# Performance work log

Hardware: AMD Instinct MI355X
Metric: run time of the kernel (lower is better)

Reference implementation:

```python
import jax, jax.numpy as jnp
import numpy as np

V, EMB, DU = 32000, 256, 512   # vocab_size, embedding_dim, dec_units
B, TIN, TOUT = 32, 64, 64      # batch, max_length_input, max_length_output


def setup_inputs() -> dict:
    key = jax.random.key(0)
    ks = jax.random.split(key, 12)
    s = 0.02  # init scale for params
    return {
        "inputs": jax.random.randint(ks[0], (B, TOUT), 0, V),
        "encoder_outputs": jax.random.normal(ks[1], (B, TIN, DU), dtype=jnp.float32),
        "h0": jax.random.normal(ks[2], (B, DU), dtype=jnp.float32),
        "c0": jax.random.normal(ks[3], (B, DU), dtype=jnp.float32),
        "emb": jax.random.normal(ks[4], (V, EMB), dtype=jnp.float32) * s,
        "Wq": jax.random.normal(ks[5], (EMB, DU), dtype=jnp.float32) * s,
        "bq": jnp.zeros((DU,), jnp.float32),
        "Wx": jax.random.normal(ks[6], (DU + EMB, 4 * DU), dtype=jnp.float32) * s,
        "Wh": jax.random.normal(ks[7], (DU, 4 * DU), dtype=jnp.float32) * s,
        "b_lstm": jnp.zeros((4 * DU,), jnp.float32),
        "Wfc": jax.random.normal(ks[8], (DU, V), dtype=jnp.float32) * s,
        "bfc": jnp.zeros((V,), jnp.float32),
    }


def _lstm(lstm_in, h0, c0, Wx, Wh, b):
    # lstm_in: [B, T, D]; keras LSTMCell gate order: i, f, g(cell), o
    def step(carry, xt):
        h, c = carry
        z = xt @ Wx + h @ Wh + b  # [B, 4*DU]
        i, f, g, o = jnp.split(z, 4, axis=-1)
        c = jax.nn.sigmoid(f) * c + jax.nn.sigmoid(i) * jnp.tanh(g)
        h = jax.nn.sigmoid(o) * jnp.tanh(c)
        return (h, c), h
    (h, c), hs = jax.lax.scan(step, (h0, c0), jnp.swapaxes(lstm_in, 0, 1))
    return jnp.swapaxes(hs, 0, 1), h, c  # [B, T, DU], [B, DU], [B, DU]


def reference(inputs, encoder_outputs, h0, c0, emb, Wq, bq, Wx, Wh, b_lstm, Wfc, bfc):
    x = emb[inputs]                                       # [B, Tout, EMB]
    q = x @ Wq + bq                                       # Luong query  [B, Tout, DU]
    scores = jnp.einsum('btd,bsd->bts', q, encoder_outputs)  # dot-product attention
    attn_w = jax.nn.softmax(scores, axis=-1)              # [B, Tout, Tin]
    att = jnp.einsum('bts,bsd->btd', attn_w, encoder_outputs)  # [B, Tout, DU]
    lstm_in = jnp.concatenate([att, x], axis=-1)          # [B, Tout, DU+EMB]
    hs, state_h, state_c = _lstm(lstm_in, h0, c0, Wx, Wh, b_lstm)
    logits = hs @ Wfc + bfc                               # [B, Tout, V]
    return logits, (state_h, state_c), attn_w
```

## Files before the change

### kernel.cpp

```cpp
#include <hip/hip_runtime.h>
#include <cstdint>

#define NB 32
#define TIN 64
#define TOUT 64
#define EMB 256
#define DU 512
#define VSZ 32000
#define BT 2048
#define G4 2048
#define KL 768

typedef __attribute__((ext_vector_type(4))) float f32x4;
typedef __attribute__((ext_vector_type(8))) short s16x8;

__device__ __forceinline__ unsigned short f2bf(float f){
  unsigned int u = __float_as_uint(f);
  u += 0x7fffu + ((u >> 16) & 1u);
  return (unsigned short)(u >> 16);
}

__global__ void k_embed(const int* __restrict__ toks, const float* __restrict__ emb,
                        unsigned short* __restrict__ x_bf, unsigned short* __restrict__ lstmin){
  int idx = blockIdx.x * 256 + threadIdx.x;
  int row = idx >> 8, e = idx & 255;
  int tok = toks[row];
  unsigned short h = f2bf(emb[tok * EMB + e]);
  x_bf[row * EMB + e] = h;
  lstmin[row * KL + DU + e] = h;
}

__global__ void k_h0cast(const float* __restrict__ h0, unsigned short* __restrict__ hbuf){
  int i = blockIdx.x * 256 + threadIdx.x;
  hbuf[i] = f2bf(h0[i]);
}

__global__ void k_enccast(const float* __restrict__ enc, unsigned short* __restrict__ enc_bf,
                          unsigned short* __restrict__ encT){
  int b = blockIdx.z, dt = blockIdx.x, st = blockIdx.y;
  __shared__ float tile[32][33];
  int tx = threadIdx.x & 31, ty = threadIdx.x >> 5;
  const float* eb = enc + b * TIN * DU;
  #pragma unroll
  for (int i = 0; i < 4; i++){
    int s = st*32 + ty + i*8, d = dt*32 + tx;
    float v = eb[s * DU + d];
    tile[ty + i*8][tx] = v;
    enc_bf[(b * TIN + s) * DU + d] = f2bf(v);
  }
  __syncthreads();
  #pragma unroll
  for (int i = 0; i < 4; i++){
    int d = dt*32 + ty + i*8, s = st*32 + tx;
    encT[(b * DU + d) * TIN + s] = f2bf(tile[tx][ty + i*8]);
  }
}

__global__ void k_transpose(const float* __restrict__ in, unsigned short* __restrict__ out, int R, int C){
  __shared__ float tile[32][33];
  int tx = threadIdx.x & 31, ty = threadIdx.x >> 5;
  int c0 = blockIdx.x * 32, r0 = blockIdx.y * 32;
  #pragma unroll
  for (int i = 0; i < 4; i++) tile[ty + i*8][tx] = in[(r0 + ty + i*8) * C + c0 + tx];
  __syncthreads();
  #pragma unroll
  for (int i = 0; i < 4; i++) out[(c0 + ty + i*8) * R + r0 + tx] = f2bf(tile[tx][ty + i*8]);
}

template<bool OUT_BF16, bool BIAS>
__global__ __launch_bounds__(256) void k_gemm_bt(const unsigned short* __restrict__ A,
                                                 const unsigned short* __restrict__ Bt,
                                                 const float* __restrict__ bias,
                                                 void* __restrict__ Cout, int M, int N, int K){
  __shared__ unsigned short As[128][72];
  __shared__ unsigned short Bs[128][72];
  const int tid = threadIdx.x;
  const int wave = tid >> 6, lane = tid & 63;
  const int l15 = lane & 15, quad = lane >> 4;
  const int m_base = blockIdx.y * 128, n_base = blockIdx.x * 128;
  const int wr = wave >> 1, wc = wave & 1;
  f32x4 acc[4][4] = {};
  const int srow = tid >> 3, schunk = (tid & 7) * 8;
  for (int k0 = 0; k0 < K; k0 += 64){
    #pragma unroll
    for (int rr = 0; rr < 4; rr++){
      int r = rr * 32 + srow;
      *(s16x8*)&As[r][schunk] = *(const s16x8*)&A[(size_t)(m_base + r) * K + k0 + schunk];
      *(s16x8*)&Bs[r][schunk] = *(const s16x8*)&Bt[(size_t)(n_base + r) * K + k0 + schunk];
    }
    __syncthreads();
    #pragma unroll
    for (int ks = 0; ks < 2; ks++){
      s16x8 af[4], bfm[4];
      #pragma unroll
      for (int mt = 0; mt < 4; mt++) af[mt]  = *(const s16x8*)&As[wr*64 + mt*16 + l15][ks*32 + quad*8];
      #pragma unroll
      for (int nt = 0; nt < 4; nt++) bfm[nt] = *(const s16x8*)&Bs[wc*64 + nt*16 + l15][ks*32 + quad*8];
      #pragma unroll
      for (int mt = 0; mt < 4; mt++)
        #pragma unroll
        for (int nt = 0; nt < 4; nt++)
          acc[mt][nt] = __builtin_amdgcn_mfma_f32_16x16x32_bf16(af[mt], bfm[nt], acc[mt][nt], 0, 0, 0);
    }
    __syncthreads();
  }
  #pragma unroll
  for (int mt = 0; mt < 4; mt++){
    #pragma unroll
    for (int nt = 0; nt < 4; nt++){
      int n = n_base + wc*64 + nt*16 + l15;
      float bv = BIAS ? bias[n] : 0.f;
      #pragma unroll
      for (int r = 0; r < 4; r++){
        int m = m_base + wr*64 + mt*16 + quad*4 + r;
        float v = acc[mt][nt][r] + bv;
        if (OUT_BF16) ((unsigned short*)Cout)[(size_t)m * N + n] = f2bf(v);
        else          ((float*)Cout)[(size_t)m * N + n] = v;
      }
    }
  }
}

__global__ __launch_bounds__(256) void k_gemm_lds(const unsigned short* __restrict__ A,
                                                  const unsigned short* __restrict__ Bt,
                                                  const float* __restrict__ bias,
                                                  float* __restrict__ Cout, int M, int N, int K){
  __shared__ unsigned short As[128 * 64];
  __shared__ unsigned short Bs[128 * 64];
  const int tid = threadIdx.x;
  const int wave = tid >> 6, lane = tid & 63;
  const int l15 = lane & 15, quad = lane >> 4;
  const int m_base = blockIdx.y * 128, n_base = blockIdx.x * 128;
  const int wr = wave >> 1, wc = wave & 1;
  f32x4 acc[4][4] = {};
  const int srow = lane >> 3;
  const int scol = (lane & 7) * 8;
  for (int k0 = 0; k0 < K; k0 += 64){
    #pragma unroll
    for (int i = 0; i < 4; i++){
      int ra = wave * 32 + i * 8;
      const unsigned short* ga = &A [(size_t)(m_base + ra + srow) * K + k0 + scol];
      const unsigned short* gb = &Bt[(size_t)(n_base + ra + srow) * K + k0 + scol];
      __builtin_amdgcn_global_load_lds((const __attribute__((address_space(1))) unsigned int*)ga,
                                       (__attribute__((address_space(3))) unsigned int*)&As[ra * 64],
                                       16, 0, 0);
      __builtin_amdgcn_global_load_lds((const __attribute__((address_space(1))) unsigned int*)gb,
                                       (__attribute__((address_space(3))) unsigned int*)&Bs[ra * 64],
                                       16, 0, 0);
    }
    __syncthreads();
    #pragma unroll
    for (int ks = 0; ks < 2; ks++){
      s16x8 af[4], bfm[4];
      #pragma unroll
      for (int mt = 0; mt < 4; mt++) af[mt]  = *(const s16x8*)&As[(wr*64 + mt*16 + l15) * 64 + ks*32 + quad*8];
      #pragma unroll
      for (int nt = 0; nt < 4; nt++) bfm[nt] = *(const s16x8*)&Bs[(wc*64 + nt*16 + l15) * 64 + ks*32 + quad*8];
      #pragma unroll
      for (int mt = 0; mt < 4; mt++)
        #pragma unroll
        for (int nt = 0; nt < 4; nt++)
          acc[mt][nt] = __builtin_amdgcn_mfma_f32_16x16x32_bf16(af[mt], bfm[nt], acc[mt][nt], 0, 0, 0);
    }
    __syncthreads();
  }
  #pragma unroll
  for (int mt = 0; mt < 4; mt++){
    #pragma unroll
    for (int nt = 0; nt < 4; nt++){
      int n = n_base + wc*64 + nt*16 + l15;
      float bv = bias[n];
      #pragma unroll
      for (int r = 0; r < 4; r++){
        int m = m_base + wr*64 + mt*16 + quad*4 + r;
        Cout[(size_t)m * N + n] = acc[mt][nt][r] + bv;
      }
    }
  }
}

__global__ __launch_bounds__(256) void k_attn(const unsigned short* __restrict__ q,
                                              const unsigned short* __restrict__ enc_bf,
                                              const unsigned short* __restrict__ encT,
                                              float* __restrict__ attn_out,
                                              unsigned short* __restrict__ lstmin){
  const int b = blockIdx.x;
  const int tid = threadIdx.x;
  const int wave = tid >> 6, lane = tid & 63;
  const int l15 = lane & 15, quad = lane >> 4;
  __shared__ unsigned short AB[2][64][136];
  __shared__ float ss[64][66];
  __shared__ unsigned short Ps[64][72];

  f32x4 acc[4] = {};
  for (int kc = 0; kc < 4; kc++){
    int k0 = kc * 128;
    #pragma unroll
    for (int i = 0; i < 4; i++){
      int idx = i * 256 + tid;
      int row = idx >> 4, ch = (idx & 15) * 8;
      *(s16x8*)&AB[0][row][ch] = *(const s16x8*)&q[(b*64 + row) * DU + k0 + ch];
      *(s16x8*)&AB[1][row][ch] = *(const s16x8*)&enc_bf[(b*64 + row) * DU + k0 + ch];
    }
    __syncthreads();
    #pragma unroll
    for (int ks = 0; ks < 4; ks++){
      s16x8 a = *(const s16x8*)&AB[0][wave*16 + l15][ks*32 + quad*8];
      #pragma unroll
      for (int nt = 0; nt < 4; nt++){
        s16x8 bb = *(const s16x8*)&AB[1][nt*16 + l15][ks*32 + quad*8];
        acc[nt] = __builtin_amdgcn_mfma_f32_16x16x32_bf16(a, bb, acc[nt], 0, 0, 0);
      }
    }
    __syncthreads();
  }
  #pragma unroll
  for (int nt = 0; nt < 4; nt++)
    #pragma unroll
    for (int r = 0; r < 4; r++)
      ss[wave*16 + quad*4 + r][nt*16 + l15] = acc[nt][r];
  __syncthreads();
  if (tid < 64){
    float mx = -1e30f;
    for (int s = 0; s < 64; s++) mx = fmaxf(mx, ss[tid][s]);
    float sum = 0.f;
    for (int s = 0; s < 64; s++){ float e = __expf(ss[tid][s] - mx); ss[tid][s] = e; sum += e; }
    float inv = 1.f / sum;
    for (int s = 0; s < 64; s++){
      float p = ss[tid][s] * inv;
      attn_out[(b*64 + tid) * 64 + s] = p;
      Ps[tid][s] = f2bf(p);
    }
  }
  __syncthreads();
  unsigned short (*B2)[72] = (unsigned short (*)[72])AB;
  for (int dc = 0; dc < 4; dc++){
    #pragma unroll
    for (int i = 0; i < 4; i++){
      int idx = i * 256 + tid;
      int row = idx >> 3, ch = (idx & 7) * 8;
      *(s16x8*)&B2[row][ch] = *(const s16x8*)&encT[(b*DU + dc*128 + row) * TIN + ch];
    }
    __syncthreads();
    f32x4 acc2[8] = {};
    #pragma unroll
    for (int ks = 0; ks < 2; ks++){
      s16x8 a = *(const s16x8*)&Ps[wave*16 + l15][ks*32 + quad*8];
      #pragma unroll
      for (int nt = 0; nt < 8; nt++){
        s16x8 bb = *(const s16x8*)&B2[nt*16 + l15][ks*32 + quad*8];
        acc2[nt] = __builtin_amdgcn_mfma_f32_16x16x32_bf16(a, bb, acc2[nt], 0, 0, 0);
      }
    }
    #pragma unroll
    for (int nt = 0; nt < 8; nt++){
      int d = dc*128 + nt*16 + l15;
      #pragma unroll
      for (int r = 0; r < 4; r++){
        int t = wave*16 + quad*4 + r;
        lstmin[(b*64 + t) * KL + d] = f2bf(acc2[nt][r]);
      }
    }
    __syncthreads();
  }
}

__global__ __launch_bounds__(512) void k_lstm(const float* __restrict__ Z,
                                              const unsigned short* __restrict__ Wh_t,
                                              const float* __restrict__ c0,
                                              unsigned short* __restrict__ hbuf,
                                              unsigned short* __restrict__ hs,
                                              float* __restrict__ out_h, float* __restrict__ out_c,
                                              unsigned int* __restrict__ cnt){
  const int wg = blockIdx.x;
  const int tid = threadIdx.x;
  const int wave = tid >> 6, lane = tid & 63;
  const int l15 = lane & 15, quad = lane >> 4;
  __shared__ unsigned short hlds[32 * 64 * 8];
  __shared__ float zs[32][132];

  const int n = wave * 16 + l15;
  const int whrow = (n >> 5) * DU + wg * 32 + (n & 31);
  s16x8 bfr[16];
  #pragma unroll
  for (int ks = 0; ks < 16; ks++)
    bfr[ks] = *(const s16x8*)&Wh_t[(size_t)whrow * DU + ks*32 + quad*8];

  const int gb = tid >> 4, gj = tid & 15;
  const int cbase = gb * DU + wg * 32 + gj;
  float c_a = c0[cbase];
  float c_b = c0[cbase + 16];

  float zv[8];
  {
    const float* zrow = Z + ((size_t)gb * 64 + 0) * G4 + wg * 32;
    #pragma unroll
    for (int g = 0; g < 4; g++){ zv[g] = zrow[g*DU + gj]; zv[4+g] = zrow[g*DU + 16 + gj]; }
  }

  for (int t = 0; t < 64; t++){
    const unsigned short* hcur = hbuf + (t & 1) * NB * DU;
    #pragma unroll
    for (int i = 0; i < 4; i++){
      int chunk = i * 512 + tid;
      int b = chunk >> 6, kc = chunk & 63;
      *(s16x8*)&hlds[(b * 64 + (kc ^ (b & 7))) * 8] = *(const s16x8*)&hcur[chunk * 8];
    }
    __syncthreads();

    f32x4 acc0 = {}, acc1 = {};
    #pragma unroll
    for (int ks = 0; ks < 16; ks++){
      int kc = ks * 4 + quad;
      int b0 = l15, b1 = 16 + l15;
      s16x8 a0 = *(const s16x8*)&hlds[(b0 * 64 + (kc ^ (b0 & 7))) * 8];
      s16x8 a1 = *(const s16x8*)&hlds[(b1 * 64 + (kc ^ (b1 & 7))) * 8];
      acc0 = __builtin_amdgcn_mfma_f32_16x16x32_bf16(a0, bfr[ks], acc0, 0, 0, 0);
      acc1 = __builtin_amdgcn_mfma_f32_16x16x32_bf16(a1, bfr[ks], acc1, 0, 0, 0);
    }
    #pragma unroll
    for (int r = 0; r < 4; r++){
      zs[quad*4 + r][wave*16 + l15]      = acc0[r];
      zs[16 + quad*4 + r][wave*16 + l15] = acc1[r];
    }
    __syncthreads();

    {
      float h_a, h_b;
      {
        float zi = zs[gb][0  + gj] + zv[0], zf = zs[gb][32 + gj] + zv[1];
        float zg = zs[gb][64 + gj] + zv[2], zo = zs[gb][96 + gj] + zv[3];
        float gi = 1.f / (1.f + __expf(-zi));
        float gf = 1.f / (1.f + __expf(-zf));
        float e2 = __expf(2.f * zg); float gc = (e2 - 1.f) / (e2 + 1.f);
        float go = 1.f / (1.f + __expf(-zo));
        c_a = gf * c_a + gi * gc;
        float ec = __expf(2.f * c_a); float tc = (ec - 1.f) / (ec + 1.f);
        h_a = go * tc;
      }
      {
        float zi = zs[gb][16  + gj] + zv[4], zf = zs[gb][48 + gj] + zv[5];
        float zg = zs[gb][80 + gj] + zv[6], zo = zs[gb][112 + gj] + zv[7];
        float gi = 1.f / (1.f + __expf(-zi));
        float gf = 1.f / (1.f + __expf(-zf));
        float e2 = __expf(2.f * zg); float gc = (e2 - 1.f) / (e2 + 1.f);
        float go = 1.f / (1.f + __expf(-zo));
        c_b = gf * c_b + gi * gc;
        float ec = __expf(2.f * c_b); float tc = (ec - 1.f) / (ec + 1.f);
        h_b = go * tc;
      }
      unsigned short ha = f2bf(h_a), hb = f2bf(h_b);
      unsigned short* hnext = hbuf + ((t + 1) & 1) * NB * DU;
      hnext[cbase] = ha;
      hnext[cbase + 16] = hb;
      size_t hsrow = ((size_t)gb * 64 + t) * DU + wg * 32 + gj;
      hs[hsrow] = ha;
      hs[hsrow + 16] = hb;
      if (t == 63){
        out_h[cbase] = h_a; out_h[cbase + 16] = h_b;
        out_c[cbase] = c_a; out_c[cbase + 16] = c_b;
      }
    }

    if (t < 63){
      const float* zrow = Z + ((size_t)gb * 64 + t + 1) * G4 + wg * 32;
      #pragma unroll
      for (int g = 0; g < 4; g++){ zv[g] = zrow[g*DU + gj]; zv[4+g] = zrow[g*DU + 16 + gj]; }
      __syncthreads();
      if (tid == 0){
        __hip_atomic_fetch_add(cnt, 1u, __ATOMIC_RELEASE, __HIP_MEMORY_SCOPE_AGENT);
        unsigned int target = 16u * (unsigned)(t + 1);
        while (__hip_atomic_load(cnt, __ATOMIC_RELAXED, __HIP_MEMORY_SCOPE_AGENT) < target)
          __builtin_amdgcn_s_sleep(1);
        __builtin_amdgcn_fence(__ATOMIC_ACQUIRE, "agent");
      }
      __syncthreads();
    }
  }
}

extern "C" void kernel_launch(void* const* d_in, const int* in_sizes, int n_in,
                              void* d_out, int out_size, void* d_ws, size_t ws_size,
                              hipStream_t stream) {
  const int*   toks   = (const int*)  d_in[0];
  const float* enc    = (const float*)d_in[1];
  const float* h0     = (const float*)d_in[2];
  const float* c0     = (const float*)d_in[3];
  const float* emb    = (const float*)d_in[4];
  const float* Wq     = (const float*)d_in[5];
  const float* bq     = (const float*)d_in[6];
  const float* Wx     = (const float*)d_in[7];
  const float* Wh     = (const float*)d_in[8];
  const float* b_lstm = (const float*)d_in[9];
  const float* Wfc    = (const float*)d_in[10];
  const float* bfc    = (const float*)d_in[11];

  float* out_logits = (float*)d_out;
  float* out_h    = out_logits + (size_t)BT * VSZ;
  float* out_c    = out_h + NB * DU;
  float* out_attn = out_c + NB * DU;

  char* ws = (char*)d_ws;
  size_t off = 0;
  auto take = [&](size_t bytes){ void* p = ws + off; off += (bytes + 255) & ~(size_t)255; return p; };
  unsigned int*   cnt    = (unsigned int*)  take(256);
  unsigned short* x_bf   = (unsigned short*)take((size_t)BT * EMB * 2);
  unsigned short* lstmin = (unsigned short*)take((size_t)BT * KL * 2);
  unsigned short* q_bf   = (unsigned short*)take((size_t)BT * DU * 2);
  unsigned short* enc_bf = (unsigned short*)take((size_t)NB * TIN * DU * 2);
  unsigned short* encT   = (unsigned short*)take((size_t)NB * DU * TIN * 2);
  unsigned short* Wq_t   = (unsigned short*)take((size_t)DU * EMB * 2);
  unsigned short* Wx_t   = (unsigned short*)take((size_t)G4 * KL * 2);
  unsigned short* Wh_t   = (unsigned short*)take((size_t)G4 * DU * 2);
  unsigned short* Wfc_t  = (unsigned short*)take((size_t)VSZ * DU * 2);
  float*          Zbuf   = (float*)         take((size_t)BT * G4 * 4);
  unsigned short* hbuf   = (unsigned short*)take((size_t)2 * NB * DU * 2);
  unsigned short* hs     = (unsigned short*)take((size_t)BT * DU * 2);

  hipMemsetAsync(cnt, 0, 256, stream);

  k_embed<<<BT * EMB / 256, 256, 0, stream>>>(toks, emb, x_bf, lstmin);
  k_h0cast<<<NB * DU / 256, 256, 0, stream>>>(h0, hbuf);
  k_enccast<<<dim3(DU/32, TIN/32, NB), 256, 0, stream>>>(enc, enc_bf, encT);
  k_transpose<<<dim3(DU/32, EMB/32), 256, 0, stream>>>(Wq, Wq_t, EMB, DU);
  k_transpose<<<dim3(G4/32, KL/32), 256, 0, stream>>>(Wx, Wx_t, KL, G4);
  k_transpose<<<dim3(G4/32, DU/32), 256, 0, stream>>>(Wh, Wh_t, DU, G4);
  k_transpose<<<dim3(VSZ/32, DU/32), 256, 0, stream>>>(Wfc, Wfc_t, DU, VSZ);

  k_gemm_bt<true, true><<<dim3(DU/128, BT/128), 256, 0, stream>>>(x_bf, Wq_t, bq, q_bf, BT, DU, EMB);
  k_attn<<<NB, 256, 0, stream>>>(q_bf, enc_bf, encT, out_attn, lstmin);
  k_gemm_bt<false, true><<<dim3(G4/128, BT/128), 256, 0, stream>>>(lstmin, Wx_t, b_lstm, Zbuf, BT, G4, KL);
  k_lstm<<<16, 512, 0, stream>>>(Zbuf, Wh_t, c0, hbuf, hs, out_h, out_c, cnt);
  k_gemm_lds<<<dim3(VSZ/128, BT/128), 256, 0, stream>>>(hs, Wfc_t, bfc, out_logits, BT, VSZ, DU);
}
```

Before: 753.1 us.

## Use cache-bypassing h exchange with relaxed barrier in LSTM; swap logits grid order

The LSTM recurrence now stages each step's hidden-state slice in LDS and writes it out as 16-byte stores with sc0 sc1 cache-bypass bits. The next step reads it back with matching bypass loads and an explicit vmcnt drain, which lets the release/acquire fences on the inter-workgroup counter be dropped. Separately, the logits GEMM grid is transposed so consecutive blocks share the same weight tile and vary over rows of hs. This reduces per-step synchronisation cost, but correctness now depends on the inline-asm cache bits giving the coherence the fences used to guarantee.

```diff
diff --git a/kernel.cpp b/kernel.cpp
--- a/kernel.cpp
+++ b/kernel.cpp
@@ -13,11 +13,24 @@
 
 typedef __attribute__((ext_vector_type(4))) float f32x4;
 typedef __attribute__((ext_vector_type(8))) short s16x8;
+typedef __attribute__((ext_vector_type(4))) unsigned int u32x4;
 
 __device__ __forceinline__ unsigned short f2bf(float f){
   unsigned int u = __float_as_uint(f);
   u += 0x7fffu + ((u >> 16) & 1u);
   return (unsigned short)(u >> 16);
+}
+
+__device__ __forceinline__ void store16_sc(void* p, u32x4 v){
+  asm volatile("global_store_dwordx4 %0, %1, off sc0 sc1" :: "v"(p), "v"(v) : "memory");
+}
+__device__ __forceinline__ u32x4 load16_sc(const void* p){
+  u32x4 r;
+  asm volatile("global_load_dwordx4 %0, %1, off sc0 sc1" : "=v"(r) : "v"(p) : "memory");
+  return r;
+}
+__device__ __forceinline__ void vm_drain(){
+  asm volatile("s_waitcnt vmcnt(0)" ::: "memory");
 }
 
 __global__ void k_embed(const int* __restrict__ toks, const float* __restrict__ emb,
@@ -130,7 +143,7 @@
   const int tid = threadIdx.x;
   const int wave = tid >> 6, lane = tid & 63;
   const int l15 = lane & 15, quad = lane >> 4;
-  const int m_base = blockIdx.y * 128, n_base = blockIdx.x * 128;
+  const int m_base = blockIdx.x * 128, n_base = blockIdx.y * 128;
   const int wr = wave >> 1, wc = wave & 1;
   f32x4 acc[4][4] = {};
   const int srow = lane >> 3;
@@ -278,6 +291,7 @@
   const int l15 = lane & 15, quad = lane >> 4;
   __shared__ unsigned short hlds[32 * 64 * 8];
   __shared__ float zs[32][132];
+  __shared__ unsigned short hstage[32 * 32];
 
   const int n = wave * 16 + l15;
   const int whrow = (n >> 5) * DU + wg * 32 + (n & 31);
@@ -291,6 +305,8 @@
   float c_a = c0[cbase];
   float c_b = c0[cbase + 16];
 
+  const int pb = tid >> 2, pch = tid & 3;
+
   float zv[8];
   {
     const float* zrow = Z + ((size_t)gb * 64 + 0) * G4 + wg * 32;
@@ -300,11 +316,15 @@
 
   for (int t = 0; t < 64; t++){
     const unsigned short* hcur = hbuf + (t & 1) * NB * DU;
+    u32x4 hv[4];
+    #pragma unroll
+    for (int i = 0; i < 4; i++) hv[i] = load16_sc(&hcur[(i * 512 + tid) * 8]);
+    vm_drain();
     #pragma unroll
     for (int i = 0; i < 4; i++){
       int chunk = i * 512 + tid;
       int b = chunk >> 6, kc = chunk & 63;
-      *(s16x8*)&hlds[(b * 64 + (kc ^ (b & 7))) * 8] = *(const s16x8*)&hcur[chunk * 8];
+      *(u32x4*)&hlds[(b * 64 + (kc ^ (b & 7))) * 8] = hv[i];
     }
     __syncthreads();
 
@@ -349,18 +369,24 @@
         float ec = __expf(2.f * c_b); float tc = (ec - 1.f) / (ec + 1.f);
         h_b = go * tc;
       }
-      unsigned short ha = f2bf(h_a), hb = f2bf(h_b);
-      unsigned short* hnext = hbuf + ((t + 1) & 1) * NB * DU;
-      hnext[cbase] = ha;
-      hnext[cbase + 16] = hb;
-      size_t hsrow = ((size_t)gb * 64 + t) * DU + wg * 32 + gj;
-      hs[hsrow] = ha;
-      hs[hsrow + 16] = hb;
+      hstage[gb * 32 + gj]      = f2bf(h_a);
+      hstage[gb * 32 + 16 + gj] = f2bf(h_b);
       if (t == 63){
         out_h[cbase] = h_a; out_h[cbase + 16] = h_b;
         out_c[cbase] = c_a; out_c[cbase + 16] = c_b;
       }
     }
+    __syncthreads();
+
+    if (tid < 128){
+      u32x4 v = *(const u32x4*)&hstage[pb * 32 + pch * 8];
+      if (t < 63){
+        unsigned short* hnext = hbuf + ((t + 1) & 1) * NB * DU;
+        store16_sc(&hnext[pb * DU + wg * 32 + pch * 8], v);
+      }
+      *(u32x4*)&hs[((size_t)pb * 64 + t) * DU + wg * 32 + pch * 8] = v;
+      vm_drain();
+    }
 
     if (t < 63){
       const float* zrow = Z + ((size_t)gb * 64 + t + 1) * G4 + wg * 32;
@@ -368,11 +394,10 @@
       for (int g = 0; g < 4; g++){ zv[g] = zrow[g*DU + gj]; zv[4+g] = zrow[g*DU + 16 + gj]; }
       __syncthreads();
       if (tid == 0){
-        __hip_atomic_fetch_add(cnt, 1u, __ATOMIC_RELEASE, __HIP_MEMORY_SCOPE_AGENT);
+        __hip_atomic_fetch_add(cnt, 1u, __ATOMIC_RELAXED, __HIP_MEMORY_SCOPE_AGENT);
         unsigned int target = 16u * (unsigned)(t + 1);
         while (__hip_atomic_load(cnt, __ATOMIC_RELAXED, __HIP_MEMORY_SCOPE_AGENT) < target)
           __builtin_amdgcn_s_sleep(1);
-        __builtin_amdgcn_fence(__ATOMIC_ACQUIRE, "agent");
       }
       __syncthreads();
     }
@@ -431,5 +456,5 @@
   k_attn<<<NB, 256, 0, stream>>>(q_bf, enc_bf, encT, out_attn, lstmin);
   k_gemm_bt<false, true><<<dim3(G4/128, BT/128), 256, 0, stream>>>(lstmin, Wx_t, b_lstm, Zbuf, BT, G4, KL);
   k_lstm<<<16, 512, 0, stream>>>(Zbuf, Wh_t, c0, hbuf, hs, out_h, out_c, cnt);
-  k_gemm_lds<<<dim3(VSZ/128, BT/128), 256, 0, stream>>>(hs, Wfc_t, bfc, out_logits, BT, VSZ, DU);
-}
+  k_gemm_lds<<<dim3(BT/128, VSZ/128), 256, 0, stream>>>(hs, Wfc_t, bfc, out_logits, BT, VSZ, DU);
+}
```

New measurement: 745.1 us. About the same (-1.1%).
